# Performance work log

Measured on AMD Instinct MI355X. Metric: run time of the kernel, lower is better.

Reference implementation:

```python
import jax, jax.numpy as jnp
import numpy as np

R = 8        # num relations (canonical etypes)
N = 50000    # num nodes (single node type)
E = 400000   # edges per relation
D = 128      # h_dim / embed_size
C = 16       # num_classes
B = 4        # num_bases


def setup_inputs() -> dict:
    key = jax.random.key(0)
    ks = jax.random.split(key, 10)
    edge_src = jax.random.randint(ks[0], (R, E), 0, N)
    edge_dst = jax.random.randint(ks[1], (R, E), 0, N)
    # xavier-uniform-ish init scale (gain for relu ~ sqrt(2))
    def xav(k, shape):
        fan_in, fan_out = shape[-2], shape[-1]
        lim = np.sqrt(2.0) * np.sqrt(6.0 / (fan_in + fan_out))
        return jax.random.uniform(k, shape, jnp.float32, -lim, lim)
    embeds = xav(ks[2], (R, N, D))          # one embed table per relation
    emb_bias = jnp.zeros((D,), jnp.float32)
    w1_basis = xav(ks[3], (B, D, D))
    w1_comp = xav(ks[4], (R, B))
    b1 = jnp.zeros((D,), jnp.float32)
    w2_basis = xav(ks[5], (B, D, C))
    w2_comp = xav(ks[6], (R, B))
    b2 = jnp.zeros((C,), jnp.float32)
    return {"edge_src": edge_src, "edge_dst": edge_dst, "embeds": embeds,
            "emb_bias": emb_bias, "w1_basis": w1_basis, "w1_comp": w1_comp,
            "b1": b1, "w2_basis": w2_basis, "w2_comp": w2_comp, "b2": b2}


def _inv_deg(edge_dst):
    # per-relation in-degree, mean with zero-degree -> 0 (DGL semantics)
    def one(dst):
        deg = jax.ops.segment_sum(jnp.ones((E,), jnp.float32), dst, num_segments=N)
        return 1.0 / jnp.maximum(deg, 1.0)
    return jax.vmap(one)(edge_dst)  # [R, N]


def _mean_agg(src_feat_r, src, dst, inv_r):
    # copy_u + mean for one relation: gather src features, segment-sum to dst, divide by degree
    msg = src_feat_r[src]                                   # [E, D']
    s = jax.ops.segment_sum(msg, dst, num_segments=N)       # [N, D']
    return s * inv_r[:, None]


def reference(edge_src, edge_dst, embeds, emb_bias, w1_basis, w1_comp, b1,
              w2_basis, w2_comp, b2):
    inv = _inv_deg(edge_dst)  # [R, N]

    # --- embed layer: per-relation embedding table, mean-agg, sum over relations ---
    h = jnp.zeros((N, D), embeds.dtype)
    for r in range(R):
        h = h + _mean_agg(embeds[r], edge_src[r], edge_dst[r], inv[r])
    h = jax.nn.relu(h + emb_bias)

    # --- hidden RGCN layer (basis regularizer, relu) ---
    W1 = jnp.einsum('rb,bio->rio', w1_comp, w1_basis)  # [R, D, D]
    h1 = jnp.zeros((N, D), h.dtype)
    for r in range(R):
        xr = h @ W1[r]                                  # per-relation transform [N, D]
        h1 = h1 + _mean_agg(xr, edge_src[r], edge_dst[r], inv[r])
    h1 = jax.nn.relu(h1 + b1)

    # --- output RGCN layer (no activation) ---
    W2 = jnp.einsum('rb,bio->rio', w2_comp, w2_basis)  # [R, D, C]
    h2 = jnp.zeros((N, C), h1.dtype)
    for r in range(R):
        xr = h1 @ W2[r]
        h2 = h2 + _mean_agg(xr, edge_src[r], edge_dst[r], inv[r])
    return h2 + b2  # torch.cat over the single node type == [N, C]
```

## Files before the change

### kernel.cpp

```cpp
#include <hip/hip_runtime.h>
#include <hip/hip_bf16.h>

#define NREL 8
#define NNODE 50000
#define NEDGE 400000
#define DIM 128
#define NCLS 16
#define NBAS 4

#define NBUCK 391
#define CAP 2048
#define MCAP 10240
#define CHUNK 8192

typedef __attribute__((ext_vector_type(8))) short short8v;
typedef __attribute__((ext_vector_type(4))) float f32x4;

__device__ __forceinline__ float bflo(unsigned int p) {
    union { unsigned int i; float f; } c; c.i = p << 16; return c.f;
}
__device__ __forceinline__ float bfhi(unsigned int p) {
    union { unsigned int i; float f; } c; c.i = p & 0xFFFF0000u; return c.f;
}
__device__ __forceinline__ unsigned short f2bf(float f) {
    union { float f; unsigned int i; } c; c.f = f;
    unsigned int r = c.i + 0x7FFFu + ((c.i >> 16) & 1u);
    return (unsigned short)(r >> 16);
}
__device__ __forceinline__ unsigned int pack2bf(float x, float y) {
    return (unsigned int)f2bf(x) | ((unsigned int)f2bf(y) << 16);
}



__global__ __launch_bounds__(512) void binA_kernel(
        const int* __restrict__ src, const int* __restrict__ dst,
        int* __restrict__ gcnt, unsigned int* __restrict__ gbuf) {
    __shared__ int cntA[NBUCK];
    __shared__ int exclA[NBUCK];
    __shared__ int gposA[NBUCK];
    __shared__ int arr[512];
    __shared__ unsigned int lbuf[CHUNK];
    int tid = threadIdx.x;
    int r = blockIdx.y;
    int base = blockIdx.x * CHUNK;
    for (int b = tid; b < NBUCK; b += 512) cntA[b] = 0;
    __syncthreads();
    unsigned int vals[16];
    int boffs[16];
    #pragma unroll
    for (int i = 0; i < 16; ++i) {
        int e = base + tid + i * 512;
        vals[i] = 0u; boffs[i] = -1;
        if (e < NEDGE) {
            int d = dst[(size_t)r * NEDGE + e];
            int s = src[(size_t)r * NEDGE + e];
            int b = d >> 7;
            int off = atomicAdd(&cntA[b], 1);
            vals[i] = (unsigned int)s | ((unsigned int)(d & 127) << 16);
            boffs[i] = (b << 13) | off;
        }
    }
    __syncthreads();
    int c = (tid < NBUCK) ? cntA[tid] : 0;
    arr[tid] = c;
    __syncthreads();
    int x = c;
    for (int off = 1; off < 512; off <<= 1) {
        int t = (tid >= off) ? arr[tid - off] : 0;
        __syncthreads();
        x += t; arr[tid] = x;
        __syncthreads();
    }
    if (tid < NBUCK) exclA[tid] = x - c;
    __syncthreads();
    #pragma unroll
    for (int i = 0; i < 16; ++i) {
        if (boffs[i] >= 0) {
            int b = boffs[i] >> 13, off = boffs[i] & 8191;
            lbuf[exclA[b] + off] = vals[i];
        }
    }
    if (tid < NBUCK) gposA[tid] = atomicAdd(&gcnt[r * NBUCK + tid], c);
    __syncthreads();
    int wave = tid >> 6, lane = tid & 63;
    for (int b = wave; b < NBUCK; b += 8) {
        int cb = cntA[b];
        int lb = exclA[b];
        int gp = gposA[b];
        if (gp + cb > CAP) cb = (CAP > gp) ? (CAP - gp) : 0;
        size_t gbo = ((size_t)(r * NBUCK + b)) * CAP + gp;
        for (int i = lane; i < cb; i += 64) gbuf[gbo + i] = lbuf[lb + i];
    }
}


__global__ __launch_bounds__(512) void merged_scan_kernel(
        const int* __restrict__ gcnt, int* __restrict__ bbase, int* __restrict__ rpA) {
    __shared__ int arr[512];
    int tid = threadIdx.x;
    int c = 0;
    if (tid < NBUCK) {
        #pragma unroll
        for (int r = 0; r < NREL; ++r) {
            int v = gcnt[r * NBUCK + tid];
            c += (v > CAP) ? CAP : v;
        }
        if (c > MCAP) c = MCAP;
    }
    arr[tid] = c;
    __syncthreads();
    int x = c;
    for (int off = 1; off < 512; off <<= 1) {
        int t = (tid >= off) ? arr[tid - off] : 0;
        __syncthreads();
        x += t; arr[tid] = x;
        __syncthreads();
    }
    if (tid < NBUCK) bbase[tid] = x - c;
    if (tid == 511) rpA[NNODE] = x;
}


__global__ __launch_bounds__(256) void binB_merged_kernel(
        const int* __restrict__ gcnt, const int* __restrict__ bbase,
        const unsigned int* __restrict__ gbuf,
        int* __restrict__ rpA, unsigned int* __restrict__ ew) {
    int b = blockIdx.x;
    int tid = threadIdx.x;
    __shared__ int deg[1024];
    __shared__ int cur[1024];
    __shared__ int arr[256];
    __shared__ unsigned int ebuf[MCAP];
    for (int k = tid; k < 1024; k += 256) deg[k] = 0;
    __syncthreads();
    int cnts[NREL];
    #pragma unroll
    for (int r = 0; r < NREL; ++r) {
        int v = gcnt[r * NBUCK + b];
        cnts[r] = (v > CAP) ? CAP : v;
    }
    #pragma unroll
    for (int r = 0; r < NREL; ++r) {
        const unsigned int* gb = gbuf + ((size_t)(r * NBUCK + b)) * CAP;
        for (int i = tid; i < cnts[r]; i += 256) {
            int nl = (gb[i] >> 16) & 127;
            atomicAdd(&deg[nl * 8 + r], 1);
        }
    }
    __syncthreads();
    int k0 = tid * 4;
    int s0, s1, s2, s3, tot = 0;
    s0 = tot; tot += deg[k0 + 0];
    s1 = tot; tot += deg[k0 + 1];
    s2 = tot; tot += deg[k0 + 2];
    s3 = tot; tot += deg[k0 + 3];
    arr[tid] = tot;
    __syncthreads();
    int x = tot;
    for (int off = 1; off < 256; off <<= 1) {
        int t = (tid >= off) ? arr[tid - off] : 0;
        __syncthreads();
        x += t; arr[tid] = x;
        __syncthreads();
    }
    int texcl = x - tot;
    cur[k0 + 0] = texcl + s0;
    cur[k0 + 1] = texcl + s1;
    cur[k0 + 2] = texcl + s2;
    cur[k0 + 3] = texcl + s3;
    __syncthreads();
    int base = bbase[b];
    int nodeBase = b * 128;
    if (tid < 128 && nodeBase + tid < NNODE)
        rpA[nodeBase + tid] = base + cur[tid * 8];
    __syncthreads();
    #pragma unroll
    for (int r = 0; r < NREL; ++r) {
        const unsigned int* gb = gbuf + ((size_t)(r * NBUCK + b)) * CAP;
        for (int i = tid; i < cnts[r]; i += 256) {
            unsigned int v = gb[i];
            int nl = (v >> 16) & 127;
            int key = nl * 8 + r;
            int off = atomicAdd(&cur[key], 1);
            if (off < MCAP) {
                unsigned int dg = (unsigned int)deg[key];
                if (dg > 8191u) dg = 8191u;
                ebuf[off] = (v & 0xFFFFu) | ((unsigned int)r << 16) | (dg << 19);
            }
        }
    }
    __syncthreads();
    int total = 0;
    #pragma unroll
    for (int r = 0; r < NREL; ++r) total += cnts[r];
    if (total > MCAP) total = MCAP;
    for (int i = tid; i < total; i += 256) ew[(size_t)base + i] = ebuf[i];
}


__global__ __launch_bounds__(256) void conv_bf16_kernel(
        const float* __restrict__ in, unsigned short* __restrict__ out) {
    size_t i = ((size_t)blockIdx.x * blockDim.x + threadIdx.x) * 4;
    if (i >= (size_t)NREL * NNODE * DIM) return;
    float4 v = *(const float4*)(in + i);
    union { unsigned short us[4]; uint2 u; } pk;
    pk.us[0] = f2bf(v.x); pk.us[1] = f2bf(v.y);
    pk.us[2] = f2bf(v.z); pk.us[3] = f2bf(v.w);
    *(uint2*)(out + i) = pk.u;
}


__global__ void wprep1_kernel(const float* __restrict__ w1_basis, unsigned short* __restrict__ w1T) {
    int idx = blockIdx.x * 256 + threadIdx.x;
    if (idx >= 128 * 512) return;
    int j = idx >> 9, k = idx & 511;
    w1T[idx] = f2bf(w1_basis[k * 128 + j]);
}

__global__ void wprep2_kernel(const float* __restrict__ w2_basis, const float* __restrict__ w2_comp,
                              unsigned short* __restrict__ w2T) {
    int idx = blockIdx.x * 256 + threadIdx.x;
    if (idx >= 128 * 128) return;
    int j = idx >> 7, k = idx & 127;
    float s = 0.f;
    #pragma unroll
    for (int b = 0; b < NBAS; ++b)
        s += w2_comp[(j >> 4) * NBAS + b] * w2_basis[(b * DIM + k) * NCLS + (j & 15)];
    w2T[idx] = f2bf(s);
}


__global__ __launch_bounds__(256) void embed_flat_kernel(
        const unsigned short* __restrict__ embeds, const int* __restrict__ rpA,
        const unsigned int* __restrict__ ew, const float* __restrict__ bias,
        unsigned short* __restrict__ h) {
    int wid = (blockIdx.x * blockDim.x + threadIdx.x) >> 6;
    int lane = threadIdx.x & 63;
    if (wid >= NNODE) return;
    int g = lane >> 4, c16 = lane & 15;
    int beg = rpA[wid], end = rpA[wid + 1];
    float a[8] = {0.f, 0.f, 0.f, 0.f, 0.f, 0.f, 0.f, 0.f};
    int e = beg;
    while (e < end) {
        unsigned int q0 = ew[e];
        unsigned int rel = (q0 >> 16) & 7u;
        int dg = (int)(q0 >> 19);
        int re = e + dg; if (re > end) re = end;
        const unsigned short* tab = embeds + (size_t)rel * NNODE * DIM + c16 * 8;
        float s[8] = {0.f, 0.f, 0.f, 0.f, 0.f, 0.f, 0.f, 0.f};
        int eq = e;
        #pragma unroll 2
        for (; eq + 4 <= re; eq += 4) {
            unsigned int srci = ew[eq + g] & 0xFFFFu;
            uint4 p = *(const uint4*)(tab + (size_t)srci * DIM);
            s[0] += bflo(p.x); s[1] += bfhi(p.x);
            s[2] += bflo(p.y); s[3] += bfhi(p.y);
            s[4] += bflo(p.z); s[5] += bfhi(p.z);
            s[6] += bflo(p.w); s[7] += bfhi(p.w);
        }
        if (eq + g < re) {
            unsigned int srci = ew[eq + g] & 0xFFFFu;
            uint4 p = *(const uint4*)(tab + (size_t)srci * DIM);
            s[0] += bflo(p.x); s[1] += bfhi(p.x);
            s[2] += bflo(p.y); s[3] += bfhi(p.y);
            s[4] += bflo(p.z); s[5] += bfhi(p.z);
            s[6] += bflo(p.w); s[7] += bfhi(p.w);
        }
        float w = 1.0f / (float)dg;
        #pragma unroll
        for (int k = 0; k < 8; ++k) a[k] = fmaf(w, s[k], a[k]);
        e = re;
    }
    #pragma unroll
    for (int k = 0; k < 8; ++k) {
        a[k] += __shfl_xor(a[k], 16);
        a[k] += __shfl_xor(a[k], 32);
    }
    if (g == 0) {
        float4 b0 = *(const float4*)(bias + c16 * 8);
        float4 b1 = *(const float4*)(bias + c16 * 8 + 4);
        uint4 o;
        o.x = pack2bf(fmaxf(a[0] + b0.x, 0.f), fmaxf(a[1] + b0.y, 0.f));
        o.y = pack2bf(fmaxf(a[2] + b0.z, 0.f), fmaxf(a[3] + b0.w, 0.f));
        o.z = pack2bf(fmaxf(a[4] + b1.x, 0.f), fmaxf(a[5] + b1.y, 0.f));
        o.w = pack2bf(fmaxf(a[6] + b1.z, 0.f), fmaxf(a[7] + b1.w, 0.f));
        *(uint4*)(h + (size_t)wid * DIM + c16 * 8) = o;
    }
}


__global__ __launch_bounds__(256) void agg1_flat_kernel(
        const unsigned short* __restrict__ feat, const int* __restrict__ rpA,
        const unsigned int* __restrict__ ew, const float* __restrict__ comp,
        unsigned short* __restrict__ z) {
    __shared__ float compS[32];
    if (threadIdx.x < 32) compS[threadIdx.x] = comp[threadIdx.x];
    __syncthreads();
    int wid = (blockIdx.x * blockDim.x + threadIdx.x) >> 6;
    int lane = threadIdx.x & 63;
    if (wid >= NNODE) return;
    int g = lane >> 4, c16 = lane & 15;
    int beg = rpA[wid], end = rpA[wid + 1];
    const unsigned short* tab = feat + c16 * 8;
    float a[4][8];
    #pragma unroll
    for (int b = 0; b < 4; ++b)
        #pragma unroll
        for (int k = 0; k < 8; ++k) a[b][k] = 0.f;
    int e = beg;
    while (e < end) {
        unsigned int q0 = ew[e];
        unsigned int rel = (q0 >> 16) & 7u;
        int dg = (int)(q0 >> 19);
        int re = e + dg; if (re > end) re = end;
        float s[8] = {0.f, 0.f, 0.f, 0.f, 0.f, 0.f, 0.f, 0.f};
        int eq = e;
        #pragma unroll 2
        for (; eq + 4 <= re; eq += 4) {
            unsigned int srci = ew[eq + g] & 0xFFFFu;
            uint4 p = *(const uint4*)(tab + (size_t)srci * DIM);
            s[0] += bflo(p.x); s[1] += bfhi(p.x);
            s[2] += bflo(p.y); s[3] += bfhi(p.y);
            s[4] += bflo(p.z); s[5] += bfhi(p.z);
            s[6] += bflo(p.w); s[7] += bfhi(p.w);
        }
        if (eq + g < re) {
            unsigned int srci = ew[eq + g] & 0xFFFFu;
            uint4 p = *(const uint4*)(tab + (size_t)srci * DIM);
            s[0] += bflo(p.x); s[1] += bfhi(p.x);
            s[2] += bflo(p.y); s[3] += bfhi(p.y);
            s[4] += bflo(p.z); s[5] += bfhi(p.z);
            s[6] += bflo(p.w); s[7] += bfhi(p.w);
        }
        float w = 1.0f / (float)dg;
        unsigned int r4 = rel << 2;
        float w0 = w * compS[r4], w1 = w * compS[r4 + 1];
        float w2 = w * compS[r4 + 2], w3 = w * compS[r4 + 3];
        #pragma unroll
        for (int k = 0; k < 8; ++k) {
            a[0][k] = fmaf(w0, s[k], a[0][k]);
            a[1][k] = fmaf(w1, s[k], a[1][k]);
            a[2][k] = fmaf(w2, s[k], a[2][k]);
            a[3][k] = fmaf(w3, s[k], a[3][k]);
        }
        e = re;
    }
    #pragma unroll
    for (int b = 0; b < 4; ++b)
        #pragma unroll
        for (int k = 0; k < 8; ++k) {
            a[b][k] += __shfl_xor(a[b][k], 16);
            a[b][k] += __shfl_xor(a[b][k], 32);
        }
    if (g == 0) {
        unsigned short* zp = z + (size_t)wid * (NBAS * DIM) + c16 * 8;
        #pragma unroll
        for (int b = 0; b < 4; ++b) {
            uint4 o;
            o.x = pack2bf(a[b][0], a[b][1]);
            o.y = pack2bf(a[b][2], a[b][3]);
            o.z = pack2bf(a[b][4], a[b][5]);
            o.w = pack2bf(a[b][6], a[b][7]);
            *(uint4*)(zp + b * 128) = o;
        }
    }
}


__global__ __launch_bounds__(256) void gemm1_mfma_kernel(
        const unsigned short* __restrict__ A, const unsigned short* __restrict__ BT,
        const float* __restrict__ bias, unsigned short* __restrict__ C, int M) {
    const int K = 512;
    __shared__ short As[128 * 40];
    __shared__ short Bs[128 * 40];
    int t = threadIdx.x;
    int row0 = blockIdx.x * 128;
    int w = t >> 6, l = t & 63;
    int wrow = w * 32;
    f32x4 acc[2][8];
    f32x4 z4 = {0.f, 0.f, 0.f, 0.f};
    #pragma unroll
    for (int mi = 0; mi < 2; ++mi)
        #pragma unroll
        for (int nj = 0; nj < 8; ++nj) acc[mi][nj] = z4;

    for (int k0 = 0; k0 < K; k0 += 32) {
        #pragma unroll
        for (int i = 0; i < 2; ++i) {
            int chunk = t + i * 256;
            int row = chunk >> 2, kc = chunk & 3;
            int gr = row0 + row;
            short8v v = {0, 0, 0, 0, 0, 0, 0, 0};
            if (gr < M) v = *(const short8v*)(A + (size_t)gr * K + k0 + kc * 8);
            *(short8v*)(&As[row * 40 + kc * 8]) = v;
            short8v u = *(const short8v*)(BT + (size_t)row * K + k0 + kc * 8);
            *(short8v*)(&Bs[row * 40 + kc * 8]) = u;
        }
        __syncthreads();
        short8v a0 = *(const short8v*)(&As[(wrow + (l & 15)) * 40 + (l >> 4) * 8]);
        short8v a1 = *(const short8v*)(&As[(wrow + 16 + (l & 15)) * 40 + (l >> 4) * 8]);
        #pragma unroll
        for (int nj = 0; nj < 8; ++nj) {
            short8v b = *(const short8v*)(&Bs[(nj * 16 + (l & 15)) * 40 + (l >> 4) * 8]);
            acc[0][nj] = __builtin_amdgcn_mfma_f32_16x16x32_bf16(a0, b, acc[0][nj], 0, 0, 0);
            acc[1][nj] = __builtin_amdgcn_mfma_f32_16x16x32_bf16(a1, b, acc[1][nj], 0, 0, 0);
        }
        __syncthreads();
    }
    #pragma unroll
    for (int mi = 0; mi < 2; ++mi) {
        #pragma unroll
        for (int jr = 0; jr < 4; ++jr) {
            int gr = row0 + wrow + mi * 16 + (l >> 4) * 4 + jr;
            if (gr < M) {
                #pragma unroll
                for (int nj = 0; nj < 8; ++nj) {
                    int col = nj * 16 + (l & 15);
                    float v = acc[mi][nj][jr] + bias[col];
                    C[(size_t)gr * 128 + col] = f2bf(fmaxf(v, 0.f));
                }
            }
        }
    }
}


__global__ __launch_bounds__(256) void gemm2_mfma_kernel(
        const unsigned short* __restrict__ A, const unsigned short* __restrict__ BT,
        unsigned short* __restrict__ T2, int M) {
    const int K = 128;
    __shared__ short As[128 * 40];
    __shared__ short Bs[128 * 40];
    int t = threadIdx.x;
    int row0 = blockIdx.x * 128;
    int w = t >> 6, l = t & 63;
    int wrow = w * 32;
    f32x4 acc[2][8];
    f32x4 z4 = {0.f, 0.f, 0.f, 0.f};
    #pragma unroll
    for (int mi = 0; mi < 2; ++mi)
        #pragma unroll
        for (int nj = 0; nj < 8; ++nj) acc[mi][nj] = z4;

    for (int k0 = 0; k0 < K; k0 += 32) {
        #pragma unroll
        for (int i = 0; i < 2; ++i) {
            int chunk = t + i * 256;
            int row = chunk >> 2, kc = chunk & 3;
            int gr = row0 + row;
            short8v v = {0, 0, 0, 0, 0, 0, 0, 0};
            if (gr < M) v = *(const short8v*)(A + (size_t)gr * K + k0 + kc * 8);
            *(short8v*)(&As[row * 40 + kc * 8]) = v;
            short8v u = *(const short8v*)(BT + (size_t)row * K + k0 + kc * 8);
            *(short8v*)(&Bs[row * 40 + kc * 8]) = u;
        }
        __syncthreads();
        short8v a0 = *(const short8v*)(&As[(wrow + (l & 15)) * 40 + (l >> 4) * 8]);
        short8v a1 = *(const short8v*)(&As[(wrow + 16 + (l & 15)) * 40 + (l >> 4) * 8]);
        #pragma unroll
        for (int nj = 0; nj < 8; ++nj) {
            short8v b = *(const short8v*)(&Bs[(nj * 16 + (l & 15)) * 40 + (l >> 4) * 8]);
            acc[0][nj] = __builtin_amdgcn_mfma_f32_16x16x32_bf16(a0, b, acc[0][nj], 0, 0, 0);
            acc[1][nj] = __builtin_amdgcn_mfma_f32_16x16x32_bf16(a1, b, acc[1][nj], 0, 0, 0);
        }
        __syncthreads();
    }
    #pragma unroll
    for (int mi = 0; mi < 2; ++mi) {
        #pragma unroll
        for (int jr = 0; jr < 4; ++jr) {
            int gr = row0 + wrow + mi * 16 + (l >> 4) * 4 + jr;
            if (gr < M) {
                #pragma unroll
                for (int nj = 0; nj < 8; ++nj) {
                    T2[((size_t)nj * NNODE + gr) * NCLS + (l & 15)] = f2bf(acc[mi][nj][jr]);
                }
            }
        }
    }
}


__global__ __launch_bounds__(256) void agg2_flat_kernel(
        const unsigned short* __restrict__ T2, const int* __restrict__ rpA,
        const unsigned int* __restrict__ ew, const float* __restrict__ b2,
        float* __restrict__ out) {
    int wid = (blockIdx.x * blockDim.x + threadIdx.x) >> 6;
    int lane = threadIdx.x & 63;
    if (wid >= NNODE) return;
    int q = lane >> 3, il = lane & 7;
    int beg = rpA[wid], end = rpA[wid + 1];
    const unsigned short* tab = T2 + il * 2;
    float sx = 0.f, sy = 0.f;
    for (int e = beg + q; e < end; e += 8) {
        unsigned int qq = ew[e];
        float w = __builtin_amdgcn_rcpf((float)(qq >> 19));
        size_t grow = (size_t)(((qq >> 16) & 7u) * NNODE + (qq & 0xFFFFu));
        unsigned int p = *(const unsigned int*)(tab + grow * NCLS);
        sx = fmaf(w, bflo(p), sx);
        sy = fmaf(w, bfhi(p), sy);
    }
    sx += __shfl_xor(sx, 8);  sy += __shfl_xor(sy, 8);
    sx += __shfl_xor(sx, 16); sy += __shfl_xor(sy, 16);
    sx += __shfl_xor(sx, 32); sy += __shfl_xor(sy, 32);
    if (lane < 8) {
        float2 o;
        o.x = sx + b2[il * 2];
        o.y = sy + b2[il * 2 + 1];
        *(float2*)(out + (size_t)wid * NCLS + il * 2) = o;
    }
}


extern "C" void kernel_launch(void* const* d_in, const int* in_sizes, int n_in,
                              void* d_out, int out_size, void* d_ws, size_t ws_size,
                              hipStream_t stream) {
    const int* edge_src   = (const int*)d_in[0];
    const int* edge_dst   = (const int*)d_in[1];
    const float* embeds   = (const float*)d_in[2];
    const float* emb_bias = (const float*)d_in[3];
    const float* w1_basis = (const float*)d_in[4];
    const float* w1_comp  = (const float*)d_in[5];
    const float* b1       = (const float*)d_in[6];
    const float* w2_basis = (const float*)d_in[7];
    const float* w2_comp  = (const float*)d_in[8];
    const float* b2       = (const float*)d_in[9];
    float* out            = (float*)d_out;

    char* ws = (char*)d_ws;
    size_t off = 0;
    auto take = [&](size_t bytes) {
        char* p = ws + off;
        off += (bytes + 255) & ~(size_t)255;
        return p;
    };
    int* gcnt    = (int*)take((size_t)NREL * NBUCK * 4);
    int* bbase   = (int*)take((size_t)NBUCK * 4);
    int* rpA     = (int*)take((size_t)(NNODE + 1) * 4);
    unsigned int* ewAll = (unsigned int*)take((size_t)NREL * NEDGE * 4);
    unsigned short* h   = (unsigned short*)take((size_t)NNODE * DIM * 2);
    unsigned short* w1T = (unsigned short*)take((size_t)128 * 512 * 2);
    unsigned short* w2T = (unsigned short*)take((size_t)128 * 128 * 2);
    char* big    = take((size_t)NREL * NNODE * DIM * 2);
    unsigned int* gbuf = (unsigned int*)big;
    unsigned short* embeds_bf = (unsigned short*)big;
    unsigned short* z  = (unsigned short*)big;
    unsigned short* T2 = (unsigned short*)(big + (size_t)NNODE * NBAS * DIM * 2);
    unsigned short* h1 = (unsigned short*)(big + (size_t)NNODE * NBAS * DIM * 2 + (size_t)NREL * NNODE * NCLS * 2);

    hipMemsetAsync(gcnt, 0, (size_t)NREL * NBUCK * 4, stream);

    binA_kernel<<<dim3((NEDGE + CHUNK - 1) / CHUNK, NREL), 512, 0, stream>>>(
        edge_src, edge_dst, gcnt, gbuf);
    merged_scan_kernel<<<1, 512, 0, stream>>>(gcnt, bbase, rpA);
    binB_merged_kernel<<<NBUCK, 256, 0, stream>>>(gcnt, bbase, gbuf, rpA, ewAll);

    size_t embN = (size_t)NREL * NNODE * DIM;
    conv_bf16_kernel<<<(int)((embN / 4 + 255) / 256), 256, 0, stream>>>(embeds, embeds_bf);
    wprep1_kernel<<<(128 * 512 + 255) / 256, 256, 0, stream>>>(w1_basis, w1T);
    wprep2_kernel<<<(128 * 128 + 255) / 256, 256, 0, stream>>>(w2_basis, w2_comp, w2T);

    int aggBlocks = (NNODE * 64 + 255) / 256;
    embed_flat_kernel<<<aggBlocks, 256, 0, stream>>>(embeds_bf, rpA, ewAll, emb_bias, h);

    agg1_flat_kernel<<<aggBlocks, 256, 0, stream>>>(h, rpA, ewAll, w1_comp, z);
    int gemmBlocks = (NNODE + 127) / 128;
    gemm1_mfma_kernel<<<gemmBlocks, 256, 0, stream>>>(z, w1T, b1, h1, NNODE);

    gemm2_mfma_kernel<<<gemmBlocks, 256, 0, stream>>>(h1, w2T, T2, NNODE);
    agg2_flat_kernel<<<aggBlocks, 256, 0, stream>>>(T2, rpA, ewAll, b2, out);
}
```

Before: 464.9 us.

## Reorder hidden layer to transform per relation then aggregate

The hidden RGCN layer is reordered. Before, it aggregated h into four basis-weighted accumulators (an N×512 buffer) and then ran a K=512 GEMM. Now it first computes per-relation weight matrices W1[r] from the basis and coefficients, runs a batched per-relation GEMM to produce Y[r] = h·W1[r], and reuses the embed-layer aggregation kernel to mean-aggregate Y with bias and ReLU. This drops the four-accumulator gather kernel and the wide intermediate. In exchange it doubles the GEMM work, writes an 8×N×128 intermediate, and gathers from a table eight times larger than h, which caches less well.

```diff
diff --git a/kernel.cpp b/kernel.cpp
--- a/kernel.cpp
+++ b/kernel.cpp
@@ -211,11 +211,16 @@
 }
 
 
-__global__ void wprep1_kernel(const float* __restrict__ w1_basis, unsigned short* __restrict__ w1T) {
+__global__ void wprep1c_kernel(const float* __restrict__ w1_basis, const float* __restrict__ w1_comp,
+                               unsigned short* __restrict__ w1cT) {
     int idx = blockIdx.x * 256 + threadIdx.x;
-    if (idx >= 128 * 512) return;
-    int j = idx >> 9, k = idx & 511;
-    w1T[idx] = f2bf(w1_basis[k * 128 + j]);
+    if (idx >= NREL * DIM * DIM) return;
+    int r = idx >> 14, j = (idx >> 7) & 127, k = idx & 127;
+    float s = 0.f;
+    #pragma unroll
+    for (int b = 0; b < NBAS; ++b)
+        s += w1_comp[r * NBAS + b] * w1_basis[(b * DIM + k) * DIM + j];
+    w1cT[idx] = f2bf(s);
 }
 
 __global__ void wprep2_kernel(const float* __restrict__ w2_basis, const float* __restrict__ w2_comp,
@@ -231,10 +236,10 @@
 }
 
 
-__global__ __launch_bounds__(256) void embed_flat_kernel(
-        const unsigned short* __restrict__ embeds, const int* __restrict__ rpA,
+__global__ __launch_bounds__(256) void agg_relu_kernel(
+        const unsigned short* __restrict__ table, const int* __restrict__ rpA,
         const unsigned int* __restrict__ ew, const float* __restrict__ bias,
-        unsigned short* __restrict__ h) {
+        unsigned short* __restrict__ out) {
     int wid = (blockIdx.x * blockDim.x + threadIdx.x) >> 6;
     int lane = threadIdx.x & 63;
     if (wid >= NNODE) return;
@@ -247,7 +252,7 @@
         unsigned int rel = (q0 >> 16) & 7u;
         int dg = (int)(q0 >> 19);
         int re = e + dg; if (re > end) re = end;
-        const unsigned short* tab = embeds + (size_t)rel * NNODE * DIM + c16 * 8;
+        const unsigned short* tab = table + (size_t)rel * NNODE * DIM + c16 * 8;
         float s[8] = {0.f, 0.f, 0.f, 0.f, 0.f, 0.f, 0.f, 0.f};
         int eq = e;
         #pragma unroll 2
@@ -279,99 +284,24 @@
     }
     if (g == 0) {
         float4 b0 = *(const float4*)(bias + c16 * 8);
-        float4 b1 = *(const float4*)(bias + c16 * 8 + 4);
+        float4 b1v = *(const float4*)(bias + c16 * 8 + 4);
         uint4 o;
         o.x = pack2bf(fmaxf(a[0] + b0.x, 0.f), fmaxf(a[1] + b0.y, 0.f));
         o.y = pack2bf(fmaxf(a[2] + b0.z, 0.f), fmaxf(a[3] + b0.w, 0.f));
-        o.z = pack2bf(fmaxf(a[4] + b1.x, 0.f), fmaxf(a[5] + b1.y, 0.f));
-        o.w = pack2bf(fmaxf(a[6] + b1.z, 0.f), fmaxf(a[7] + b1.w, 0.f));
-        *(uint4*)(h + (size_t)wid * DIM + c16 * 8) = o;
-    }
-}
-
-
-__global__ __launch_bounds__(256) void agg1_flat_kernel(
-        const unsigned short* __restrict__ feat, const int* __restrict__ rpA,
-        const unsigned int* __restrict__ ew, const float* __restrict__ comp,
-        unsigned short* __restrict__ z) {
-    __shared__ float compS[32];
-    if (threadIdx.x < 32) compS[threadIdx.x] = comp[threadIdx.x];
-    __syncthreads();
-    int wid = (blockIdx.x * blockDim.x + threadIdx.x) >> 6;
-    int lane = threadIdx.x & 63;
-    if (wid >= NNODE) return;
-    int g = lane >> 4, c16 = lane & 15;
-    int beg = rpA[wid], end = rpA[wid + 1];
-    const unsigned short* tab = feat + c16 * 8;
-    float a[4][8];
-    #pragma unroll
-    for (int b = 0; b < 4; ++b)
-        #pragma unroll
-        for (int k = 0; k < 8; ++k) a[b][k] = 0.f;
-    int e = beg;
-    while (e < end) {
-        unsigned int q0 = ew[e];
-        unsigned int rel = (q0 >> 16) & 7u;
-        int dg = (int)(q0 >> 19);
-        int re = e + dg; if (re > end) re = end;
-        float s[8] = {0.f, 0.f, 0.f, 0.f, 0.f, 0.f, 0.f, 0.f};
-        int eq = e;
-        #pragma unroll 2
-        for (; eq + 4 <= re; eq += 4) {
-            unsigned int srci = ew[eq + g] & 0xFFFFu;
-            uint4 p = *(const uint4*)(tab + (size_t)srci * DIM);
-            s[0] += bflo(p.x); s[1] += bfhi(p.x);
-            s[2] += bflo(p.y); s[3] += bfhi(p.y);
-            s[4] += bflo(p.z); s[5] += bfhi(p.z);
-            s[6] += bflo(p.w); s[7] += bfhi(p.w);
-        }
-        if (eq + g < re) {
-            unsigned int srci = ew[eq + g] & 0xFFFFu;
-            uint4 p = *(const uint4*)(tab + (size_t)srci * DIM);
-            s[0] += bflo(p.x); s[1] += bfhi(p.x);
-            s[2] += bflo(p.y); s[3] += bfhi(p.y);
-            s[4] += bflo(p.z); s[5] += bfhi(p.z);
-            s[6] += bflo(p.w); s[7] += bfhi(p.w);
-        }
-        float w = 1.0f / (float)dg;
-        unsigned int r4 = rel << 2;
-        float w0 = w * compS[r4], w1 = w * compS[r4 + 1];
-        float w2 = w * compS[r4 + 2], w3 = w * compS[r4 + 3];
-        #pragma unroll
-        for (int k = 0; k < 8; ++k) {
-            a[0][k] = fmaf(w0, s[k], a[0][k]);
-            a[1][k] = fmaf(w1, s[k], a[1][k]);
-            a[2][k] = fmaf(w2, s[k], a[2][k]);
-            a[3][k] = fmaf(w3, s[k], a[3][k]);
-        }
-        e = re;
-    }
-    #pragma unroll
-    for (int b = 0; b < 4; ++b)
-        #pragma unroll
-        for (int k = 0; k < 8; ++k) {
-            a[b][k] += __shfl_xor(a[b][k], 16);
-            a[b][k] += __shfl_xor(a[b][k], 32);
-        }
-    if (g == 0) {
-        unsigned short* zp = z + (size_t)wid * (NBAS * DIM) + c16 * 8;
-        #pragma unroll
-        for (int b = 0; b < 4; ++b) {
-            uint4 o;
-            o.x = pack2bf(a[b][0], a[b][1]);
-            o.y = pack2bf(a[b][2], a[b][3]);
-            o.z = pack2bf(a[b][4], a[b][5]);
-            o.w = pack2bf(a[b][6], a[b][7]);
-            *(uint4*)(zp + b * 128) = o;
-        }
-    }
-}
-
-
-__global__ __launch_bounds__(256) void gemm1_mfma_kernel(
-        const unsigned short* __restrict__ A, const unsigned short* __restrict__ BT,
-        const float* __restrict__ bias, unsigned short* __restrict__ C, int M) {
-    const int K = 512;
+        o.z = pack2bf(fmaxf(a[4] + b1v.x, 0.f), fmaxf(a[5] + b1v.y, 0.f));
+        o.w = pack2bf(fmaxf(a[6] + b1v.z, 0.f), fmaxf(a[7] + b1v.w, 0.f));
+        *(uint4*)(out + (size_t)wid * DIM + c16 * 8) = o;
+    }
+}
+
+
+__global__ __launch_bounds__(256) void ygemm_mfma_kernel(
+        const unsigned short* __restrict__ A, const unsigned short* __restrict__ BTall,
+        unsigned short* __restrict__ Y, int M) {
+    const int K = 128;
+    int r = blockIdx.y;
+    const unsigned short* BT = BTall + (size_t)r * DIM * K;
+    unsigned short* Yr = Y + (size_t)r * NNODE * DIM;
     __shared__ short As[128 * 40];
     __shared__ short Bs[128 * 40];
     int t = threadIdx.x;
@@ -417,8 +347,7 @@
                 #pragma unroll
                 for (int nj = 0; nj < 8; ++nj) {
                     int col = nj * 16 + (l & 15);
-                    float v = acc[mi][nj][jr] + bias[col];
-                    C[(size_t)gr * 128 + col] = f2bf(fmaxf(v, 0.f));
+                    Yr[(size_t)gr * DIM + col] = f2bf(acc[mi][nj][jr]);
                 }
             }
         }
@@ -540,14 +469,14 @@
     int* rpA     = (int*)take((size_t)(NNODE + 1) * 4);
     unsigned int* ewAll = (unsigned int*)take((size_t)NREL * NEDGE * 4);
     unsigned short* h   = (unsigned short*)take((size_t)NNODE * DIM * 2);
-    unsigned short* w1T = (unsigned short*)take((size_t)128 * 512 * 2);
-    unsigned short* w2T = (unsigned short*)take((size_t)128 * 128 * 2);
+    unsigned short* w1cT = (unsigned short*)take((size_t)NREL * DIM * DIM * 2);
+    unsigned short* w2T  = (unsigned short*)take((size_t)128 * 128 * 2);
     char* big    = take((size_t)NREL * NNODE * DIM * 2);
     unsigned int* gbuf = (unsigned int*)big;
     unsigned short* embeds_bf = (unsigned short*)big;
-    unsigned short* z  = (unsigned short*)big;
+    unsigned short* Y  = (unsigned short*)big;
     unsigned short* T2 = (unsigned short*)(big + (size_t)NNODE * NBAS * DIM * 2);
-    unsigned short* h1 = (unsigned short*)(big + (size_t)NNODE * NBAS * DIM * 2 + (size_t)NREL * NNODE * NCLS * 2);
+    unsigned short* h1 = h;
 
     hipMemsetAsync(gcnt, 0, (size_t)NREL * NBUCK * 4, stream);
 
@@ -558,15 +487,15 @@
 
     size_t embN = (size_t)NREL * NNODE * DIM;
     conv_bf16_kernel<<<(int)((embN / 4 + 255) / 256), 256, 0, stream>>>(embeds, embeds_bf);
-    wprep1_kernel<<<(128 * 512 + 255) / 256, 256, 0, stream>>>(w1_basis, w1T);
+    wprep1c_kernel<<<(NREL * DIM * DIM + 255) / 256, 256, 0, stream>>>(w1_basis, w1_comp, w1cT);
     wprep2_kernel<<<(128 * 128 + 255) / 256, 256, 0, stream>>>(w2_basis, w2_comp, w2T);
 
     int aggBlocks = (NNODE * 64 + 255) / 256;
-    embed_flat_kernel<<<aggBlocks, 256, 0, stream>>>(embeds_bf, rpA, ewAll, emb_bias, h);
-
-    agg1_flat_kernel<<<aggBlocks, 256, 0, stream>>>(h, rpA, ewAll, w1_comp, z);
+    agg_relu_kernel<<<aggBlocks, 256, 0, stream>>>(embeds_bf, rpA, ewAll, emb_bias, h);
+
     int gemmBlocks = (NNODE + 127) / 128;
-    gemm1_mfma_kernel<<<gemmBlocks, 256, 0, stream>>>(z, w1T, b1, h1, NNODE);
+    ygemm_mfma_kernel<<<dim3(gemmBlocks, NREL), 256, 0, stream>>>(h, w1cT, Y, NNODE);
+    agg_relu_kernel<<<aggBlocks, 256, 0, stream>>>(Y, rpA, ewAll, b1, h1);
 
     gemm2_mfma_kernel<<<gemmBlocks, 256, 0, stream>>>(h1, w2T, T2, NNODE);
     agg2_flat_kernel<<<aggBlocks, 256, 0, stream>>>(T2, rpA, ewAll, b2, out);
```

After: 477.3 us. 2.6% more time.

## Fold bf16 conversion and weight prep into binning kernels to cut launches

Applied to the files above, without the earlier changes.

Extra blocks are appended to the edge-binning kernel so it converts the first 75% of the embedding table to bf16 in the same launch. The two weight-prep kernels become extra blocks of the second binning kernel. The gbuf scratch is moved past the converted region so both can coexist, and a separate kernel converts the remaining tail. This removes three launches and lets the conversion overlap the low-occupancy binning work, at the cost of more complex buffer aliasing and hardcoded sizes.

```diff
diff --git a/kernel.cpp b/kernel.cpp
--- a/kernel.cpp
+++ b/kernel.cpp
@@ -12,6 +12,10 @@
 #define CAP 2048
 #define MCAP 10240
 #define CHUNK 8192
+#define NCHUNKS 49
+#define NBINA (NCHUNKS * NREL)
+#define TOTELEM (51200000)
+#define SPLITELEM (38400000)
 
 typedef __attribute__((ext_vector_type(8))) short short8v;
 typedef __attribute__((ext_vector_type(4))) float f32x4;
@@ -33,17 +37,28 @@
 
 
 
-__global__ __launch_bounds__(512) void binA_kernel(
+__global__ __launch_bounds__(512) void k1_kernel(
         const int* __restrict__ src, const int* __restrict__ dst,
-        int* __restrict__ gcnt, unsigned int* __restrict__ gbuf) {
+        int* __restrict__ gcnt, unsigned int* __restrict__ gbuf,
+        const float* __restrict__ embeds, unsigned short* __restrict__ embeds_bf) {
     __shared__ int cntA[NBUCK];
     __shared__ int exclA[NBUCK];
     __shared__ int gposA[NBUCK];
     __shared__ int arr[512];
     __shared__ unsigned int lbuf[CHUNK];
     int tid = threadIdx.x;
-    int r = blockIdx.y;
-    int base = blockIdx.x * CHUNK;
+    int bid = blockIdx.x;
+    if (bid >= NBINA) {
+        size_t i = (size_t)(bid - NBINA) * 2048 + (size_t)tid * 4;
+        float4 v = *(const float4*)(embeds + i);
+        union { unsigned short us[4]; uint2 u; } pk;
+        pk.us[0] = f2bf(v.x); pk.us[1] = f2bf(v.y);
+        pk.us[2] = f2bf(v.z); pk.us[3] = f2bf(v.w);
+        *(uint2*)(embeds_bf + i) = pk.u;
+        return;
+    }
+    int r = bid / NCHUNKS;
+    int base = (bid % NCHUNKS) * CHUNK;
     for (int b = tid; b < NBUCK; b += 512) cntA[b] = 0;
     __syncthreads();
     unsigned int vals[16];
@@ -122,16 +137,36 @@
 }
 
 
-__global__ __launch_bounds__(256) void binB_merged_kernel(
+__global__ __launch_bounds__(256) void k2_kernel(
         const int* __restrict__ gcnt, const int* __restrict__ bbase,
         const unsigned int* __restrict__ gbuf,
-        int* __restrict__ rpA, unsigned int* __restrict__ ew) {
-    int b = blockIdx.x;
-    int tid = threadIdx.x;
+        int* __restrict__ rpA, unsigned int* __restrict__ ew,
+        const float* __restrict__ w1_basis, unsigned short* __restrict__ w1T,
+        const float* __restrict__ w2_basis, const float* __restrict__ w2_comp,
+        unsigned short* __restrict__ w2T) {
     __shared__ int deg[1024];
     __shared__ int cur[1024];
     __shared__ int arr[256];
     __shared__ unsigned int ebuf[MCAP];
+    int tid = threadIdx.x;
+    int bid = blockIdx.x;
+    if (bid >= NBUCK) {
+        if (bid < NBUCK + 256) {
+            int idx = (bid - NBUCK) * 256 + tid;
+            int j = idx >> 9, k = idx & 511;
+            w1T[idx] = f2bf(w1_basis[k * 128 + j]);
+        } else {
+            int idx = (bid - NBUCK - 256) * 256 + tid;
+            int j = idx >> 7, k = idx & 127;
+            float s = 0.f;
+            #pragma unroll
+            for (int b = 0; b < NBAS; ++b)
+                s += w2_comp[(j >> 4) * NBAS + b] * w2_basis[(b * DIM + k) * NCLS + (j & 15)];
+            w2T[idx] = f2bf(s);
+        }
+        return;
+    }
+    int b = bid;
     for (int k = tid; k < 1024; k += 256) deg[k] = 0;
     __syncthreads();
     int cnts[NREL];
@@ -199,10 +234,9 @@
 }
 
 
-__global__ __launch_bounds__(256) void conv_bf16_kernel(
+__global__ __launch_bounds__(256) void k3_conv_kernel(
         const float* __restrict__ in, unsigned short* __restrict__ out) {
-    size_t i = ((size_t)blockIdx.x * blockDim.x + threadIdx.x) * 4;
-    if (i >= (size_t)NREL * NNODE * DIM) return;
+    size_t i = (size_t)SPLITELEM + (size_t)blockIdx.x * 1024 + (size_t)threadIdx.x * 4;
     float4 v = *(const float4*)(in + i);
     union { unsigned short us[4]; uint2 u; } pk;
     pk.us[0] = f2bf(v.x); pk.us[1] = f2bf(v.y);
@@ -211,30 +245,10 @@
 }
 
 
-__global__ void wprep1_kernel(const float* __restrict__ w1_basis, unsigned short* __restrict__ w1T) {
-    int idx = blockIdx.x * 256 + threadIdx.x;
-    if (idx >= 128 * 512) return;
-    int j = idx >> 9, k = idx & 511;
-    w1T[idx] = f2bf(w1_basis[k * 128 + j]);
-}
-
-__global__ void wprep2_kernel(const float* __restrict__ w2_basis, const float* __restrict__ w2_comp,
-                              unsigned short* __restrict__ w2T) {
-    int idx = blockIdx.x * 256 + threadIdx.x;
-    if (idx >= 128 * 128) return;
-    int j = idx >> 7, k = idx & 127;
-    float s = 0.f;
-    #pragma unroll
-    for (int b = 0; b < NBAS; ++b)
-        s += w2_comp[(j >> 4) * NBAS + b] * w2_basis[(b * DIM + k) * NCLS + (j & 15)];
-    w2T[idx] = f2bf(s);
-}
-
-
-__global__ __launch_bounds__(256) void embed_flat_kernel(
-        const unsigned short* __restrict__ embeds, const int* __restrict__ rpA,
+__global__ __launch_bounds__(256) void agg_relu_kernel(
+        const unsigned short* __restrict__ table, const int* __restrict__ rpA,
         const unsigned int* __restrict__ ew, const float* __restrict__ bias,
-        unsigned short* __restrict__ h) {
+        unsigned short* __restrict__ out) {
     int wid = (blockIdx.x * blockDim.x + threadIdx.x) >> 6;
     int lane = threadIdx.x & 63;
     if (wid >= NNODE) return;
@@ -247,7 +261,7 @@
         unsigned int rel = (q0 >> 16) & 7u;
         int dg = (int)(q0 >> 19);
         int re = e + dg; if (re > end) re = end;
-        const unsigned short* tab = embeds + (size_t)rel * NNODE * DIM + c16 * 8;
+        const unsigned short* tab = table + (size_t)rel * NNODE * DIM + c16 * 8;
         float s[8] = {0.f, 0.f, 0.f, 0.f, 0.f, 0.f, 0.f, 0.f};
         int eq = e;
         #pragma unroll 2
@@ -279,13 +293,13 @@
     }
     if (g == 0) {
         float4 b0 = *(const float4*)(bias + c16 * 8);
-        float4 b1 = *(const float4*)(bias + c16 * 8 + 4);
+        float4 b1v = *(const float4*)(bias + c16 * 8 + 4);
         uint4 o;
         o.x = pack2bf(fmaxf(a[0] + b0.x, 0.f), fmaxf(a[1] + b0.y, 0.f));
         o.y = pack2bf(fmaxf(a[2] + b0.z, 0.f), fmaxf(a[3] + b0.w, 0.f));
-        o.z = pack2bf(fmaxf(a[4] + b1.x, 0.f), fmaxf(a[5] + b1.y, 0.f));
-        o.w = pack2bf(fmaxf(a[6] + b1.z, 0.f), fmaxf(a[7] + b1.w, 0.f));
-        *(uint4*)(h + (size_t)wid * DIM + c16 * 8) = o;
+        o.z = pack2bf(fmaxf(a[4] + b1v.x, 0.f), fmaxf(a[5] + b1v.y, 0.f));
+        o.w = pack2bf(fmaxf(a[6] + b1v.z, 0.f), fmaxf(a[7] + b1v.w, 0.f));
+        *(uint4*)(out + (size_t)wid * DIM + c16 * 8) = o;
     }
 }
 
@@ -543,26 +557,23 @@
     unsigned short* w1T = (unsigned short*)take((size_t)128 * 512 * 2);
     unsigned short* w2T = (unsigned short*)take((size_t)128 * 128 * 2);
     char* big    = take((size_t)NREL * NNODE * DIM * 2);
-    unsigned int* gbuf = (unsigned int*)big;
     unsigned short* embeds_bf = (unsigned short*)big;
+    unsigned int* gbuf = (unsigned int*)(big + (size_t)SPLITELEM * 2);
     unsigned short* z  = (unsigned short*)big;
     unsigned short* T2 = (unsigned short*)(big + (size_t)NNODE * NBAS * DIM * 2);
     unsigned short* h1 = (unsigned short*)(big + (size_t)NNODE * NBAS * DIM * 2 + (size_t)NREL * NNODE * NCLS * 2);
 
     hipMemsetAsync(gcnt, 0, (size_t)NREL * NBUCK * 4, stream);
 
-    binA_kernel<<<dim3((NEDGE + CHUNK - 1) / CHUNK, NREL), 512, 0, stream>>>(
-        edge_src, edge_dst, gcnt, gbuf);
+    k1_kernel<<<NBINA + 18750, 512, 0, stream>>>(edge_src, edge_dst, gcnt, gbuf,
+                                                 embeds, embeds_bf);
     merged_scan_kernel<<<1, 512, 0, stream>>>(gcnt, bbase, rpA);
-    binB_merged_kernel<<<NBUCK, 256, 0, stream>>>(gcnt, bbase, gbuf, rpA, ewAll);
-
-    size_t embN = (size_t)NREL * NNODE * DIM;
-    conv_bf16_kernel<<<(int)((embN / 4 + 255) / 256), 256, 0, stream>>>(embeds, embeds_bf);
-    wprep1_kernel<<<(128 * 512 + 255) / 256, 256, 0, stream>>>(w1_basis, w1T);
-    wprep2_kernel<<<(128 * 128 + 255) / 256, 256, 0, stream>>>(w2_basis, w2_comp, w2T);
+    k2_kernel<<<NBUCK + 256 + 64, 256, 0, stream>>>(gcnt, bbase, gbuf, rpA, ewAll,
+                                                    w1_basis, w1T, w2_basis, w2_comp, w2T);
+    k3_conv_kernel<<<12500, 256, 0, stream>>>(embeds, embeds_bf);
 
     int aggBlocks = (NNODE * 64 + 255) / 256;
-    embed_flat_kernel<<<aggBlocks, 256, 0, stream>>>(embeds_bf, rpA, ewAll, emb_bias, h);
+    agg_relu_kernel<<<aggBlocks, 256, 0, stream>>>(embeds_bf, rpA, ewAll, emb_bias, h);
 
     agg1_flat_kernel<<<aggBlocks, 256, 0, stream>>>(h, rpA, ewAll, w1_comp, z);
     int gemmBlocks = (NNODE + 127) / 128;
```

After: 441.9 us. 1.05x faster.
